# Kernel tuning notes

Hardware: AMD Instinct MI355X
Metric: run time of the kernel (lower is better)

## Reference

```python
import jax, jax.numpy as jnp
import numpy as np

B, A, C, H, W = 4, 6, 80, 128, 128
INPUT_SHIFT = 4
IMG = 1024.0
K_PRE = 4095            # kSRamSize: pre-NMS candidate budget
POST_K = 300            # post_nms_top_k
THR_INT = 1             # ceil(0.05 * 2**INPUT_SHIFT)
NMS_THR = 128.0 / 256.0 # ceil(0.5 * 2**kNmsThresholdShift) / 2**8
MARGIN_INT = 0          # ceil(0.0 * 2**INPUT_SHIFT)
CLASS_OFFSET = 0
NEG = -(1 << 30)
OUT_SHIFT = 2           # kOutputBBoxShift


def setup_inputs() -> dict:
    key = jax.random.key(0)
    k1, = jax.random.split(key, 1)
    # quantized int8 repr (scale 1/2**4) of box deltas + class scores
    data = jax.random.randint(k1, (B, A * (4 + C), H, W), -128, 128, dtype=jnp.int32)
    # grid anchors: centers at stride 8, per-anchor square sizes
    stride = IMG / H
    ys, xs = np.meshgrid(np.arange(H), np.arange(W), indexing="ij")
    cx = ((xs + 0.5) * stride).astype(np.float32)
    cy = ((ys + 0.5) * stride).astype(np.float32)
    half = (32.0 * (1.33 ** np.arange(A, dtype=np.float32)))[:, None, None] / 2.0
    anchor = np.stack([cx[None] - half, cy[None] - half, cx[None] + half, cy[None] + half], axis=1)
    # exp table exactly as _gen_exp_table with in_scale = 1/2**INPUT_SHIFT
    idx = np.arange(-128, 128, dtype=np.float32) / (1 << INPUT_SHIFT)
    ev = np.exp(idx)
    bit_num = float(np.ceil(np.log2(ev.max() + 1.0)))
    exp_shift = int(max(15 - bit_num, INPUT_SHIFT))
    exp_table = np.round(ev * (1 << exp_shift)).astype(np.int32)
    return {"data": data, "anchor": jnp.asarray(anchor, jnp.float32),
            "exp_table": jnp.asarray(exp_table), "exp_shift": exp_shift}


def _decode(data, anchor, exp_table, exp_shift):
    d = data.reshape(B, A, 4 + C, H, W)
    deltas = jnp.transpose(d[:, :, :4], (0, 1, 3, 4, 2)).reshape(B, -1, 4)   # [B,N,4] int
    cls = jnp.transpose(d[:, :, 4:], (0, 1, 3, 4, 2)).reshape(B, -1, C)      # [B,N,C] int
    score = cls.max(-1)                                   # int, scale 1/2**4
    label = jnp.argmax(cls, -1).astype(jnp.int32) + CLASS_OFFSET
    anc = jnp.transpose(anchor, (0, 2, 3, 1)).reshape(-1, 4)                 # [N,4] matches (A,H,W)
    aw = anc[:, 2] - anc[:, 0]
    ah = anc[:, 3] - anc[:, 1]
    acx = (anc[:, 0] + anc[:, 2]) * 0.5
    acy = (anc[:, 1] + anc[:, 3]) * 0.5
    inv = 1.0 / (1 << INPUT_SHIFT)
    dx = deltas[..., 0].astype(jnp.float32) * inv
    dy = deltas[..., 1].astype(jnp.float32) * inv
    esc = 1.0 / (1 << exp_shift)
    ew = exp_table[jnp.clip(deltas[..., 2], -128, 127) + 128].astype(jnp.float32) * esc
    eh = exp_table[jnp.clip(deltas[..., 3], -128, 127) + 128].astype(jnp.float32) * esc
    pcx = acx + dx * aw
    pcy = acy + dy * ah
    pw = aw * ew
    ph = ah * eh
    boxes = jnp.stack([pcx - pw * 0.5, pcy - ph * 0.5, pcx + pw * 0.5, pcy + ph * 0.5], -1)
    return jnp.clip(boxes, 0.0, IMG), score, label       # use_clippings


def _iou(b):  # [K,4] -> [K,K]
    area = jnp.maximum(b[:, 2] - b[:, 0], 0.0) * jnp.maximum(b[:, 3] - b[:, 1], 0.0)
    lt = jnp.maximum(b[:, None, :2], b[None, :, :2])
    rb = jnp.minimum(b[:, None, 2:], b[None, :, 2:])
    wh = jnp.maximum(rb - lt, 0.0)
    inter = wh[..., 0] * wh[..., 1]
    return inter / jnp.maximum(area[:, None] + area[None, :] - inter, 1e-6)


def _nms(boxes, scores, labels):
    # boxes/scores are pre-sorted by descending score
    sup = (_iou(boxes) > NMS_THR) \
          & (labels[:, None] == labels[None, :]) \
          & ((scores[:, None] - scores[None, :]) >= MARGIN_INT)
    valid = scores > NEG
    idx = jnp.arange(K_PRE)

    def body(i, keep):
        sup_i = sup[i] & (idx > i)
        return jnp.where(keep[i] & valid[i], keep & jnp.logical_not(sup_i), keep)

    return jax.lax.fori_loop(0, K_PRE, body, valid)


def reference(data, anchor, exp_table, exp_shift):
    boxes, score, label = _decode(data, anchor, exp_table, exp_shift)
    ms = jnp.where(score >= THR_INT, score, NEG)          # box_filter_threshold
    topv, topi = jax.lax.top_k(ms, K_PRE)                 # [B,K]
    boxes_k = jnp.take_along_axis(boxes, topi[:, :, None], axis=1)
    labels_k = jnp.take_along_axis(label, topi, axis=1)
    keep = jax.vmap(_nms)(boxes_k, topv, labels_k)
    fs = jnp.where(keep, topv, NEG)
    outv, outi = jax.lax.top_k(fs, POST_K)
    out_boxes = jnp.take_along_axis(boxes_k, outi[:, :, None], axis=1)
    out_labels = jnp.take_along_axis(labels_k, outi, axis=1)
    out_boxes_i = jnp.round(out_boxes * (1 << OUT_SHIFT)).astype(jnp.int32)  # qint16 @ kOutputBBoxShift
    return out_boxes_i, outv.astype(jnp.int32), out_labels
```

## Files before the change

### kernel.cpp

```cpp
#include <hip/hip_runtime.h>
#include <stdint.h>

#define BATCH 4
#define NA 6
#define NC 80
#define HW (128*128)
#define NPB (NA*HW)
#define KPRE 4095
#define KPAD 4096
#define POSTK 300
#define NEGV (-(1<<30))
#define NCHUNK (NPB/256)

#define OFF_BOXES    0
#define OFF_BOXK     6291456
#define OFF_MS       6553600
#define OFF_LAB      8126464
#define OFF_BCNT     9699328
#define OFF_BASE     10485760
#define OFF_SCUT     10487808
#define OFF_TOT      10487872
#define OFF_TOPV     10489920
#define OFF_LABK     10555456
#define OFF_MASK     10620992

__device__ __forceinline__ float4 dpp_decode_box(int dxi, int dyi, int dwi, int dhi,
                                                 float a0, float a1, float a2, float a3,
                                                 const int* __restrict__ exp_table, float esc) {
#pragma clang fp contract(off)
    float aw  = a2 - a0;
    float ah  = a3 - a1;
    float acx = (a0 + a2) * 0.5f;
    float acy = (a1 + a3) * 0.5f;
    float dx  = (float)dxi * 0.0625f;
    float dy  = (float)dyi * 0.0625f;
    int e2 = dwi < -128 ? -128 : (dwi > 127 ? 127 : dwi);
    int e3 = dhi < -128 ? -128 : (dhi > 127 ? 127 : dhi);
    float ew = (float)exp_table[e2 + 128] * esc;
    float eh = (float)exp_table[e3 + 128] * esc;
    float pcx = acx + dx * aw;
    float pcy = acy + dy * ah;
    float pw = aw * ew;
    float ph = ah * eh;
    float x0 = pcx - pw * 0.5f;
    float y0 = pcy - ph * 0.5f;
    float x1 = pcx + pw * 0.5f;
    float y1 = pcy + ph * 0.5f;
    x0 = fminf(fmaxf(x0, 0.f), 1024.f);
    y0 = fminf(fmaxf(y0, 0.f), 1024.f);
    x1 = fminf(fmaxf(x1, 0.f), 1024.f);
    y1 = fminf(fmaxf(y1, 0.f), 1024.f);
    return make_float4(x0, y0, x1, y1);
}

__global__ __launch_bounds__(256) void dpp_decode_kernel(
        const int* __restrict__ data, const float* __restrict__ anchor,
        const int* __restrict__ exp_table, const int* __restrict__ exp_shift_p,
        int* __restrict__ ms, int* __restrict__ labels, float4* __restrict__ boxes,
        int* __restrict__ blockcnt) {
    int b = blockIdx.z, a = blockIdx.y, tid = threadIdx.x;
    int idx = blockIdx.x * 256 + tid;
    const int4* dptr = (const int4*)(data + (size_t)(b * NA + a) * 84 * HW);

    int4 d0 = dptr[idx];
    int4 d1 = dptr[4096 + idx];
    int4 d2 = dptr[2 * 4096 + idx];
    int4 d3 = dptr[3 * 4096 + idx];

    int4 m = dptr[4 * 4096 + idx];
    int4 lab = make_int4(0, 0, 0, 0);
#pragma unroll 4
    for (int c = 1; c < NC; c++) {
        int4 v = dptr[(4 + c) * 4096 + idx];
        if (v.x > m.x) { m.x = v.x; lab.x = c; }
        if (v.y > m.y) { m.y = v.y; lab.y = c; }
        if (v.z > m.z) { m.z = v.z; lab.z = c; }
        if (v.w > m.w) { m.w = v.w; lab.w = c; }
    }

    const float4* aptr = (const float4*)(anchor + (size_t)a * 4 * HW);
    float4 ax0 = aptr[idx];
    float4 ay0 = aptr[4096 + idx];
    float4 ax1 = aptr[2 * 4096 + idx];
    float4 ay1 = aptr[3 * 4096 + idx];

    int eshift = exp_shift_p[0];
    float esc = 1.0f / (float)(1 << eshift);

    float4 box0 = dpp_decode_box(d0.x, d1.x, d2.x, d3.x, ax0.x, ay0.x, ax1.x, ay1.x, exp_table, esc);
    float4 box1 = dpp_decode_box(d0.y, d1.y, d2.y, d3.y, ax0.y, ay0.y, ax1.y, ay1.y, exp_table, esc);
    float4 box2 = dpp_decode_box(d0.z, d1.z, d2.z, d3.z, ax0.z, ay0.z, ax1.z, ay1.z, exp_table, esc);
    float4 box3 = dpp_decode_box(d0.w, d1.w, d2.w, d3.w, ax0.w, ay0.w, ax1.w, ay1.w, exp_table, esc);

    int s0 = (m.x >= 1) ? m.x : NEGV;
    int s1 = (m.y >= 1) ? m.y : NEGV;
    int s2 = (m.z >= 1) ? m.z : NEGV;
    int s3 = (m.w >= 1) ? m.w : NEGV;

    size_t nb = (size_t)b * NPB + (size_t)a * HW;
    ((int4*)ms)[(nb >> 2) + idx] = make_int4(s0, s1, s2, s3);
    ((int4*)labels)[(nb >> 2) + idx] = lab;
    boxes[nb + 4 * (size_t)idx]     = box0;
    boxes[nb + 4 * (size_t)idx + 1] = box1;
    boxes[nb + 4 * (size_t)idx + 2] = box2;
    boxes[nb + 4 * (size_t)idx + 3] = box3;

    __shared__ int hist[512];
    hist[tid] = 0;
    hist[tid + 256] = 0;
    __syncthreads();
    int q = tid >> 6;
    if (s0 >= 1) atomicAdd(&hist[q * 128 + s0], 1);
    if (s1 >= 1) atomicAdd(&hist[q * 128 + s1], 1);
    if (s2 >= 1) atomicAdd(&hist[q * 128 + s2], 1);
    if (s3 >= 1) atomicAdd(&hist[q * 128 + s3], 1);
    __syncthreads();
#pragma unroll
    for (int k = 0; k < 2; k++) {
        int lin = tid + (k << 8);
        int q2 = lin >> 7, v = lin & 127;
        int chunk = a * 64 + blockIdx.x * 4 + q2;
        blockcnt[((b << 7) + v) * NCHUNK + chunk] = hist[q2 * 128 + v];
    }
}

__global__ __launch_bounds__(384) void dpp_scan_kernel(int* __restrict__ bcnt,
                                                       int* __restrict__ tot,
                                                       int* __restrict__ topv,
                                                       int* __restrict__ labk,
                                                       float4* __restrict__ boxk) {
    int v = blockIdx.x, b = blockIdx.y, t = threadIdx.x;
    if (t < 32) {
        int slot = (b << 12) + (v << 5) + t;
        topv[slot] = NEGV;
        labk[slot] = 0;
        boxk[slot] = make_float4(0.f, 0.f, 0.f, 0.f);
    }
    int* bc = bcnt + ((b << 7) + v) * NCHUNK;
    int x = bc[t];
    int lane = t & 63, w = t >> 6;
    int s = x;
#pragma unroll
    for (int d = 1; d < 64; d <<= 1) {
        int y = __shfl_up(s, d);
        if (lane >= d) s += y;
    }
    __shared__ int wsum[6];
    if (lane == 63) wsum[w] = s;
    __syncthreads();
    int off = 0;
    for (int i = 0; i < w; i++) off += wsum[i];
    int incl = s + off;
    bc[t] = incl - x;
    if (t == NCHUNK - 1) tot[(b << 7) + v] = incl;
}

__global__ __launch_bounds__(512) void dpp_cutoff_kernel(const int* __restrict__ tot,
                                                         int* __restrict__ base,
                                                         int* __restrict__ s_cut) {
    int t = threadIdx.x;
    int b = t >> 7, v = t & 127;
    __shared__ int lds[512];
    lds[t] = tot[t];
    __syncthreads();
    if (v == 0) {
        int cum = 0, sc = 1;
        for (int vv = 127; vv >= 1; vv--) {
            base[(b << 7) + vv] = cum;
            cum += lds[(b << 7) + vv];
            sc = vv;
            if (cum >= KPRE) break;
        }
        s_cut[b] = sc;
    }
}

__global__ __launch_bounds__(256) void dpp_place_kernel(
        const int* __restrict__ ms, const int* __restrict__ labels, const float4* __restrict__ boxes,
        const int* __restrict__ blockoff, const int* __restrict__ base, const int* __restrict__ s_cut,
        int* __restrict__ topv, int* __restrict__ labk, float4* __restrict__ boxk) {
    int chunk = blockIdx.x, b = blockIdx.y, tid = threadIdx.x;
    int n = (chunk << 8) + tid;
    int s = ms[(size_t)b * NPB + n];
    __shared__ int lds_s[256];
    lds_s[tid] = s;
    __syncthreads();
    int sc = s_cut[b];
    if (s >= sc) {
        int r = 0;
#pragma unroll 4
        for (int j = 0; j < tid; j++) r += (lds_s[j] == s) ? 1 : 0;
        int pos = base[(b << 7) + s] + blockoff[((b << 7) + s) * NCHUNK + chunk] + r;
        if (pos < KPRE) {
            topv[(b << 12) + pos] = s;
            labk[(b << 12) + pos] = labels[(size_t)b * NPB + n];
            boxk[(b << 12) + pos] = boxes[(size_t)b * NPB + n];
        }
    }
}

__global__ __launch_bounds__(256) void dpp_mask_kernel(
        const float4* __restrict__ boxk, const int* __restrict__ labk,
        unsigned long long* __restrict__ mask) {
#pragma clang fp contract(off)
    int cc = blockIdx.x, rg = blockIdx.y, b = blockIdx.z;
    int t = threadIdx.x, lane = t & 63;
    int rc = (rg << 2) + (t >> 6);
    int row = (rc << 6) + lane;
    __shared__ float4 cb[64];
    __shared__ int cl[64];
    int col0 = cc << 6;
    if (t < 64) {
        cb[t] = boxk[(b << 12) + col0 + t];
        cl[t] = labk[(b << 12) + col0 + t];
    }
    __syncthreads();
    size_t mi = ((size_t)(b << 12) + row) * 64 + cc;
    if (cc < rc) {
        mask[mi] = 0ull;
        return;
    }
    float4 rbx = boxk[(b << 12) + row];
    int rl = labk[(b << 12) + row];
    float rw = fmaxf(rbx.z - rbx.x, 0.f), rh = fmaxf(rbx.w - rbx.y, 0.f);
    float ra = rw * rh;
    unsigned long long bits = 0ull;
#pragma unroll 4
    for (int j = 0; j < 64; j++) {
        float4 c = cb[j];
        float cw = fmaxf(c.z - c.x, 0.f), ch = fmaxf(c.w - c.y, 0.f);
        float ca = cw * ch;
        float lx = fmaxf(rbx.x, c.x), ly = fmaxf(rbx.y, c.y);
        float rx = fminf(rbx.z, c.z), ry = fminf(rbx.w, c.w);
        float wx = fmaxf(rx - lx, 0.f), wy = fmaxf(ry - ly, 0.f);
        float inter = wx * wy;
        float uni = fmaxf((ra + ca) - inter, 1e-6f);
        float iou = inter / uni;
        bool sup = (iou > 0.5f) && (cl[j] == rl) && ((col0 + j) > row);
        if (sup) bits |= (1ull << j);
    }
    mask[mi] = bits;
}

__global__ __launch_bounds__(64) void dpp_nms_kernel(
        const float4* __restrict__ boxk, const int* __restrict__ labk, const int* __restrict__ topv,
        const unsigned long long* __restrict__ mask, int* __restrict__ out) {
    int b = blockIdx.x, lane = threadIdx.x;
    const int* tv = topv + (b << 12);
    const unsigned long long* mrow = mask + (size_t)(b << 12) * 64;

    unsigned long long sup = 0ull;
    for (int k = 0; k < 64; k++) {
        int v = tv[(k << 6) + lane];
        unsigned long long mb = __ballot(v <= NEGV);
        if (lane == k) sup = mb;
    }

    __shared__ int keep_lds[POSTK];
    int kc = 0;
    unsigned long long w_win = __shfl(sup, 0);

    unsigned long long pl[8], pu[8];
#pragma unroll
    for (int u = 0; u < 8; u++) {
        pl[u] = mrow[(size_t)u * 64 + lane];
        pu[u] = mrow[(size_t)u * 64 + 0];
    }

    bool done = false;
    for (int ii = 0; ii < KPAD && !done; ii += 8) {
#pragma unroll
        for (int u = 0; u < 8; u++) {
            int i = ii + u;
            if (!done && i < KPRE) {
                if ((i & 63) == 0 && i != 0) w_win = __shfl(sup, i >> 6);
                if (!((w_win >> (i & 63)) & 1ull)) {
                    if (lane == 0) keep_lds[kc] = i;
                    kc++;
                    if (kc == POSTK) {
                        done = true;
                    } else {
                        sup   |= pl[u];
                        w_win |= pu[u];
                    }
                }
            }
            int r = i + 8;
            if (r > KPRE - 1) r = KPRE - 1;
            pl[u] = mrow[(size_t)r * 64 + lane];
            pu[u] = mrow[(size_t)r * 64 + (r >> 6)];
        }
    }

    int kept = kc;
    if (kc < POSTK) {
        for (int j = 0; j < KPRE && kc < POSTK; j++) {
            unsigned long long w = __shfl(sup, j >> 6);
            if ((w >> (j & 63)) & 1ull) {
                if (lane == 0) keep_lds[kc] = j;
                kc++;
            }
        }
    }
    __syncthreads();

    for (int k = lane; k < POSTK; k += 64) {
        int slot = keep_lds[k];
        float4 bx = boxk[(b << 12) + slot];
        int lb = labk[(b << 12) + slot];
        int sv = (k < kept) ? tv[slot] : NEGV;
        int o = ((b * POSTK) + k) << 2;
        out[o + 0] = (int)rintf(bx.x * 4.0f);
        out[o + 1] = (int)rintf(bx.y * 4.0f);
        out[o + 2] = (int)rintf(bx.z * 4.0f);
        out[o + 3] = (int)rintf(bx.w * 4.0f);
        out[BATCH * POSTK * 4 + b * POSTK + k] = sv;
        out[BATCH * POSTK * 5 + b * POSTK + k] = lb;
    }
}

extern "C" void kernel_launch(void* const* d_in, const int* in_sizes, int n_in,
                              void* d_out, int out_size, void* d_ws, size_t ws_size,
                              hipStream_t stream) {
    const int*   data      = (const int*)d_in[0];
    const float* anchor    = (const float*)d_in[1];
    const int*   exp_table = (const int*)d_in[2];
    const int*   exp_shift = (const int*)d_in[3];

    char* ws = (char*)d_ws;
    float4* boxes  = (float4*)(ws + OFF_BOXES);
    float4* boxk   = (float4*)(ws + OFF_BOXK);
    int*    ms     = (int*)(ws + OFF_MS);
    int*    labels = (int*)(ws + OFF_LAB);
    int*    bcnt   = (int*)(ws + OFF_BCNT);
    int*    base   = (int*)(ws + OFF_BASE);
    int*    s_cut  = (int*)(ws + OFF_SCUT);
    int*    tot    = (int*)(ws + OFF_TOT);
    int*    topv   = (int*)(ws + OFF_TOPV);
    int*    labk   = (int*)(ws + OFF_LABK);
    unsigned long long* mask = (unsigned long long*)(ws + OFF_MASK);

    dpp_decode_kernel<<<dim3(16, NA, BATCH), 256, 0, stream>>>(
        data, anchor, exp_table, exp_shift, ms, labels, boxes, bcnt);
    dpp_scan_kernel<<<dim3(128, BATCH), 384, 0, stream>>>(bcnt, tot, topv, labk, boxk);
    dpp_cutoff_kernel<<<1, 512, 0, stream>>>(tot, base, s_cut);
    dpp_place_kernel<<<dim3(NCHUNK, BATCH), 256, 0, stream>>>(
        ms, labels, boxes, bcnt, base, s_cut, topv, labk, boxk);
    dpp_mask_kernel<<<dim3(64, 16, BATCH), 256, 0, stream>>>(boxk, labk, mask);
    dpp_nms_kernel<<<BATCH, 64, 0, stream>>>(boxk, labk, topv, mask, (int*)d_out);
}
```

Baseline: 292.7 us.

## Limit NMS mask to first 1024 rows and rank ties with wave ballots

The suppression bitmask is now built only for the first 1024 candidate rows instead of all 4096, which cuts the mask kernel grid by four. The NMS kernel runs the bitmask sweep over those rows and falls back to direct IoU checks against the kept set for any later candidate when fewer than 300 boxes survive. Separately, the place kernel replaces its serial per-thread equal-score count with wave ballots plus a per-wave LDS histogram. The fallback path is serial per candidate and can be slow when it triggers, but it keeps the result exact.

Result: faster. 265.1 us (-9.4%).

```diff
diff --git a/kernel.cpp b/kernel.cpp
--- a/kernel.cpp
+++ b/kernel.cpp
@@ -11,6 +11,7 @@
 #define POSTK 300
 #define NEGV (-(1<<30))
 #define NCHUNK (NPB/256)
+#define R1 1024
 
 #define OFF_BOXES    0
 #define OFF_BOXK     6291456
@@ -53,6 +54,19 @@
     return make_float4(x0, y0, x1, y1);
 }
 
+__device__ __forceinline__ bool dpp_sup_test(float4 p, float pa, int pl_, float4 c, int cl_) {
+#pragma clang fp contract(off)
+    float cw = fmaxf(c.z - c.x, 0.f), ch = fmaxf(c.w - c.y, 0.f);
+    float ca = cw * ch;
+    float lx = fmaxf(p.x, c.x), ly = fmaxf(p.y, c.y);
+    float rx = fminf(p.z, c.z), ry = fminf(p.w, c.w);
+    float wx = fmaxf(rx - lx, 0.f), wy = fmaxf(ry - ly, 0.f);
+    float inter = wx * wy;
+    float uni = fmaxf((pa + ca) - inter, 1e-6f);
+    float iou = inter / uni;
+    return (iou > 0.5f) && (cl_ == pl_);
+}
+
 __global__ __launch_bounds__(256) void dpp_decode_kernel(
         const int* __restrict__ data, const float* __restrict__ anchor,
         const int* __restrict__ exp_table, const int* __restrict__ exp_shift_p,
@@ -180,16 +194,28 @@
         const int* __restrict__ blockoff, const int* __restrict__ base, const int* __restrict__ s_cut,
         int* __restrict__ topv, int* __restrict__ labk, float4* __restrict__ boxk) {
     int chunk = blockIdx.x, b = blockIdx.y, tid = threadIdx.x;
+    int lane = tid & 63, w = tid >> 6;
     int n = (chunk << 8) + tid;
     int s = ms[(size_t)b * NPB + n];
-    __shared__ int lds_s[256];
-    lds_s[tid] = s;
-    __syncthreads();
+
+    __shared__ int whist[512];
+    whist[tid] = 0;
+    whist[tid + 256] = 0;
+    __syncthreads();
+    if (s >= 1) atomicAdd(&whist[(w << 7) + s], 1);
+
+    unsigned long long eq = ~0ull;
+#pragma unroll
+    for (int k = 0; k < 7; k++) {
+        unsigned long long bk = __ballot((s >> k) & 1);
+        eq &= ((s >> k) & 1) ? bk : ~bk;
+    }
+    int r = __popcll(eq & ((1ull << lane) - 1ull));
+    __syncthreads();
+
     int sc = s_cut[b];
     if (s >= sc) {
-        int r = 0;
-#pragma unroll 4
-        for (int j = 0; j < tid; j++) r += (lds_s[j] == s) ? 1 : 0;
+        for (int w2 = 0; w2 < w; w2++) r += whist[(w2 << 7) + s];
         int pos = base[(b << 7) + s] + blockoff[((b << 7) + s) * NCHUNK + chunk] + r;
         if (pos < KPRE) {
             topv[(b << 12) + pos] = s;
@@ -215,7 +241,7 @@
         cl[t] = labk[(b << 12) + col0 + t];
     }
     __syncthreads();
-    size_t mi = ((size_t)(b << 12) + row) * 64 + cc;
+    size_t mi = ((size_t)b * R1 + row) * 64 + cc;
     if (cc < rc) {
         mask[mi] = 0ull;
         return;
@@ -227,16 +253,7 @@
     unsigned long long bits = 0ull;
 #pragma unroll 4
     for (int j = 0; j < 64; j++) {
-        float4 c = cb[j];
-        float cw = fmaxf(c.z - c.x, 0.f), ch = fmaxf(c.w - c.y, 0.f);
-        float ca = cw * ch;
-        float lx = fmaxf(rbx.x, c.x), ly = fmaxf(rbx.y, c.y);
-        float rx = fminf(rbx.z, c.z), ry = fminf(rbx.w, c.w);
-        float wx = fmaxf(rx - lx, 0.f), wy = fmaxf(ry - ly, 0.f);
-        float inter = wx * wy;
-        float uni = fmaxf((ra + ca) - inter, 1e-6f);
-        float iou = inter / uni;
-        bool sup = (iou > 0.5f) && (cl[j] == rl) && ((col0 + j) > row);
+        bool sup = dpp_sup_test(rbx, ra, rl, cb[j], cl[j]) && ((col0 + j) > row);
         if (sup) bits |= (1ull << j);
     }
     mask[mi] = bits;
@@ -245,9 +262,10 @@
 __global__ __launch_bounds__(64) void dpp_nms_kernel(
         const float4* __restrict__ boxk, const int* __restrict__ labk, const int* __restrict__ topv,
         const unsigned long long* __restrict__ mask, int* __restrict__ out) {
+#pragma clang fp contract(off)
     int b = blockIdx.x, lane = threadIdx.x;
     const int* tv = topv + (b << 12);
-    const unsigned long long* mrow = mask + (size_t)(b << 12) * 64;
+    const unsigned long long* mrow = mask + (size_t)b * R1 * 64;
 
     unsigned long long sup = 0ull;
     for (int k = 0; k < 64; k++) {
@@ -268,11 +286,11 @@
     }
 
     bool done = false;
-    for (int ii = 0; ii < KPAD && !done; ii += 8) {
+    for (int ii = 0; ii < R1 && !done; ii += 8) {
 #pragma unroll
         for (int u = 0; u < 8; u++) {
             int i = ii + u;
-            if (!done && i < KPRE) {
+            if (!done) {
                 if ((i & 63) == 0 && i != 0) w_win = __shfl(sup, i >> 6);
                 if (!((w_win >> (i & 63)) & 1ull)) {
                     if (lane == 0) keep_lds[kc] = i;
@@ -286,9 +304,32 @@
                 }
             }
             int r = i + 8;
-            if (r > KPRE - 1) r = KPRE - 1;
+            if (r > R1 - 1) r = R1 - 1;
             pl[u] = mrow[(size_t)r * 64 + lane];
             pu[u] = mrow[(size_t)r * 64 + (r >> 6)];
+        }
+    }
+
+    if (kc < POSTK) {
+        for (int i = R1; i < KPRE && kc < POSTK; i++) {
+            unsigned long long w = __shfl(sup, i >> 6);
+            if ((w >> (i & 63)) & 1ull) continue;
+            float4 bi = boxk[(b << 12) + i];
+            int li = labk[(b << 12) + i];
+            bool supp = false;
+            for (int k = lane; k < kc; k += 64) {
+                int j = keep_lds[k];
+                float4 c = boxk[(b << 12) + j];
+                float cw = fmaxf(c.z - c.x, 0.f), ch = fmaxf(c.w - c.y, 0.f);
+                float ca = cw * ch;
+                supp |= dpp_sup_test(c, ca, labk[(b << 12) + j], bi, li);
+            }
+            if (__ballot(supp)) {
+                if (lane == (i >> 6)) sup |= 1ull << (i & 63);
+            } else {
+                if (lane == 0) keep_lds[kc] = i;
+                kc++;
+            }
         }
     }
 
@@ -346,6 +387,6 @@
     dpp_cutoff_kernel<<<1, 512, 0, stream>>>(tot, base, s_cut);
     dpp_place_kernel<<<dim3(NCHUNK, BATCH), 256, 0, stream>>>(
         ms, labels, boxes, bcnt, base, s_cut, topv, labk, boxk);
-    dpp_mask_kernel<<<dim3(64, 16, BATCH), 256, 0, stream>>>(boxk, labk, mask);
+    dpp_mask_kernel<<<dim3(64, 4, BATCH), 256, 0, stream>>>(boxk, labk, mask);
     dpp_nms_kernel<<<BATCH, 64, 0, stream>>>(boxk, labk, topv, mask, (int*)d_out);
 }
```
